# Optimization experiments

Hardware: AMD Instinct MI355X
Metric: run time of the kernel (lower is better)

The kernel has to match this reference:

```python
import jax, jax.numpy as jnp
import numpy as np

TEMPORAL_WIDTH = 4  # hardcoded in GRUBlock


def causal_conv1d(x, w, b):
    """Depthwise causal temporal conv. x:[B,T,R], w:[4,R], b:[R].
    out[t] = sum_i w[i] * x[t - 3 + i] + b (zero left padding)."""
    T = x.shape[1]
    xp = jnp.pad(x, ((0, 0), (TEMPORAL_WIDTH - 1, 0), (0, 0)))
    y = b
    for i in range(TEMPORAL_WIDTH):  # tiny fixed loop over 4 taps
        y = y + w[i] * xp[:, i:i + T]
    return y


def linear_scan(a, b):
    """h_t = a_t * h_{t-1} + b_t with h_{-1}=0, via associative scan over time."""
    def comb(e1, e2):
        a1, b1 = e1
        a2, b2 = e2
        return a2 * a1, a2 * b1 + b2
    _, h = jax.lax.associative_scan(comb, (a, b), axis=1)
    return h


def setup_inputs() -> dict:
    key = jax.random.key(0)
    k1, k2, k3, k4 = jax.random.split(key, 4)
    B, T, H, R = 4, 8192, 1024, 1024
    x = jax.random.normal(k1, (B, T, H), dtype=jnp.float32)
    # lecun init: N(0, 1/sqrt(d_in)); torch Linear weight is [out, in]
    w_zh = jax.random.normal(k2, (2 * R, H), dtype=jnp.float32) / np.sqrt(H)
    w_out = jax.random.normal(k3, (H, R), dtype=jnp.float32) / np.sqrt(R)
    conv_w = jax.random.normal(k4, (TEMPORAL_WIDTH, R), dtype=jnp.float32) / np.sqrt(TEMPORAL_WIDTH)
    conv_b = jnp.zeros((R,), dtype=jnp.float32)
    return {"x": x, "w_zh": w_zh, "w_out": w_out, "conv_w": conv_w, "conv_b": conv_b}


def reference(x, w_zh, w_out, conv_w, conv_b):
    # residual causal conv
    x = x + causal_conv1d(x, conv_w, conv_b)
    # fused z/h projection: [B,T,H] @ [H,2R]
    zh = jnp.einsum('bth,rh->btr', x, w_zh)
    z, h = jnp.split(zh, 2, axis=-1)
    z = jax.nn.sigmoid(z)
    # GRU-style linear recurrence: h_t = (1-z_t) h_{t-1} + z_t h~_t
    h_o = linear_scan(1.0 - z, z * h)
    return jnp.einsum('btr,hr->bth', h_o, w_out)
```

## Files before the change

kernel.cpp:

```cpp
#include <hip/hip_runtime.h>

typedef __bf16 bf16x8 __attribute__((ext_vector_type(8)));
typedef __bf16 bf16x4 __attribute__((ext_vector_type(4)));
typedef float  f32x4  __attribute__((ext_vector_type(4)));

static constexpr int Bb = 4, T = 8192, H = 1024, R = 1024;
static constexpr int BT = Bb * T;
static constexpr int N1 = 2 * R;
static constexpr int CH = 64;
static constexpr int L  = T / CH;

__device__ __forceinline__ void g2lds16(const void* g, void* l) {
  __builtin_amdgcn_global_load_lds(
      (const __attribute__((address_space(1))) unsigned int*)g,
      (__attribute__((address_space(3))) unsigned int*)l, 16, 0, 0);
}

__global__ __launch_bounds__(256) void cast_f32_bf16(const float* __restrict__ in,
                                                     __bf16* __restrict__ out, int n4) {
  int i = blockIdx.x * 256 + threadIdx.x;
  if (i >= n4) return;
  const f32x4 v = *(const f32x4*)(in + (size_t)i * 4);
  bf16x4 o;
  o[0] = (__bf16)v[0]; o[1] = (__bf16)v[1]; o[2] = (__bf16)v[2]; o[3] = (__bf16)v[3];
  *(bf16x4*)(out + (size_t)i * 4) = o;
}

__global__ __launch_bounds__(256) void conv_residual_cast(const float* __restrict__ x,
                                                          const float* __restrict__ cw,
                                                          const float* __restrict__ cb,
                                                          __bf16* __restrict__ xc) {
  const size_t i4 = (size_t)blockIdx.x * 256 + threadIdx.x;
  const size_t v  = i4 * 4;
  const int    h  = (int)(v & (size_t)(H - 1));
  const size_t bt = v >> 10;
  const int    t  = (int)(bt & (size_t)(T - 1));
  f32x4 acc = *(const f32x4*)(cb + h);
  const f32x4 xv = *(const f32x4*)(x + v);
#pragma unroll
  for (int i = 0; i < 4; ++i) {
    const int tt = t - 3 + i;
    if (tt >= 0) {
      const f32x4 xi = *(const f32x4*)(x + (bt - 3 + i) * H + h);
      const f32x4 wi = *(const f32x4*)(cw + i * H + h);
      acc += wi * xi;
    }
  }
  acc += xv;
  bf16x4 o;
  o[0] = (__bf16)acc[0]; o[1] = (__bf16)acc[1]; o[2] = (__bf16)acc[2]; o[3] = (__bf16)acc[3];
  *(bf16x4*)(xc + v) = o;
}

template <typename OUT_T>
__global__ __launch_bounds__(256) void gemm_bt(const __bf16* __restrict__ A,
                                               const __bf16* __restrict__ Bm,
                                               OUT_T* __restrict__ C,
                                               int M, int N, int K) {
  __shared__ __align__(16) __bf16 sA[128 * 32];
  __shared__ __align__(16) __bf16 sB[128 * 32];
  const int tid  = threadIdx.x;
  const int wave = tid >> 6;
  const int lane = tid & 63;
  const int lr = lane & 15;
  const int lq = lane >> 4;
  const int bm0 = blockIdx.y * 128;
  const int bn0 = blockIdx.x * 128;
  const int wm = (wave >> 1) * 64;
  const int wn = (wave & 1) * 64;

  f32x4 acc[4][4] = {};

  const size_t aBase = (size_t)(bm0 + (tid >> 2)) * K + (tid & 3) * 8;
  const size_t bBase = (size_t)(bn0 + (tid >> 2)) * K + (tid & 3) * 8;
  const int ldsOff = (tid & ~63) * 8;

  for (int k0 = 0; k0 < K; k0 += 32) {
    g2lds16(A  + aBase + k0,                 sA + ldsOff);
    g2lds16(A  + aBase + (size_t)64 * K + k0, sA + ldsOff + 2048);
    g2lds16(Bm + bBase + k0,                 sB + ldsOff);
    g2lds16(Bm + bBase + (size_t)64 * K + k0, sB + ldsOff + 2048);
    __syncthreads();
    bf16x8 af[4], bfr[4];
#pragma unroll
    for (int i = 0; i < 4; ++i) {
      af[i]  = *(const bf16x8*)(sA + (wm + i * 16 + lr) * 32 + lq * 8);
      bfr[i] = *(const bf16x8*)(sB + (wn + i * 16 + lr) * 32 + lq * 8);
    }
#pragma unroll
    for (int i = 0; i < 4; ++i)
#pragma unroll
      for (int j = 0; j < 4; ++j)
        acc[i][j] = __builtin_amdgcn_mfma_f32_16x16x32_bf16(af[i], bfr[j], acc[i][j], 0, 0, 0);
    __syncthreads();
  }
#pragma unroll
  for (int i = 0; i < 4; ++i)
#pragma unroll
    for (int j = 0; j < 4; ++j) {
      const int col = bn0 + wn + j * 16 + lr;
#pragma unroll
      for (int rr = 0; rr < 4; ++rr) {
        const int row = bm0 + wm + i * 16 + lq * 4 + rr;
        C[(size_t)row * N + col] = (OUT_T)acc[i][j][rr];
      }
    }
}

__global__ __launch_bounds__(256) void scan_pass1(const __bf16* __restrict__ zh,
                                                  float* __restrict__ aggA,
                                                  float* __restrict__ aggB) {
  const int r = blockIdx.x * 256 + threadIdx.x;
  const int c = blockIdx.y;
  const int b = blockIdx.z;
  size_t base = ((size_t)b * T + (size_t)c * L) * N1 + r;
  float Aacc = 1.f, Bacc = 0.f;
#pragma unroll 4
  for (int t = 0; t < L; ++t) {
    const float s  = (float)zh[base];
    const float hh = (float)zh[base + R];
    base += N1;
    const float z = 1.f / (1.f + __expf(-s));
    const float a = 1.f - z;
    Bacc = a * Bacc + z * hh;
    Aacc *= a;
  }
  const size_t o = ((size_t)b * CH + c) * R + r;
  aggA[o] = Aacc;
  aggB[o] = Bacc;
}

__global__ __launch_bounds__(256) void scan_pass2(const float* __restrict__ aggA,
                                                  const float* __restrict__ aggB,
                                                  float* __restrict__ carry) {
  const int idx = blockIdx.x * 256 + threadIdx.x;
  const int b = idx >> 10;
  const int r = idx & (R - 1);
  float h = 0.f;
#pragma unroll 8
  for (int c = 0; c < CH; ++c) {
    const size_t o = ((size_t)b * CH + c) * R + r;
    carry[o] = h;
    h = aggA[o] * h + aggB[o];
  }
}

__global__ __launch_bounds__(256) void scan_pass3(const __bf16* __restrict__ zh,
                                                  const float* __restrict__ carry,
                                                  __bf16* __restrict__ ho) {
  const int r = blockIdx.x * 256 + threadIdx.x;
  const int c = blockIdx.y;
  const int b = blockIdx.z;
  size_t base  = ((size_t)b * T + (size_t)c * L) * N1 + r;
  size_t obase = ((size_t)b * T + (size_t)c * L) * R + r;
  float h = carry[((size_t)b * CH + c) * R + r];
#pragma unroll 4
  for (int t = 0; t < L; ++t) {
    const float s  = (float)zh[base];
    const float hh = (float)zh[base + R];
    base += N1;
    const float z = 1.f / (1.f + __expf(-s));
    h = (1.f - z) * h + z * hh;
    ho[obase] = (__bf16)h;
    obase += R;
  }
}

extern "C" void kernel_launch(void* const* d_in, const int* in_sizes, int n_in,
                              void* d_out, int out_size, void* d_ws, size_t ws_size,
                              hipStream_t stream) {
  const float* x      = (const float*)d_in[0];
  const float* w_zh   = (const float*)d_in[1];
  const float* w_out  = (const float*)d_in[2];
  const float* conv_w = (const float*)d_in[3];
  const float* conv_b = (const float*)d_in[4];
  float* out = (float*)d_out;

  char* ws = (char*)d_ws;
  size_t off = 0;
  __bf16* wzh_b  = (__bf16*)(ws + off); off += (size_t)N1 * H * 2;
  __bf16* wout_b = (__bf16*)(ws + off); off += (size_t)H * R * 2;
  __bf16* xc     = (__bf16*)(ws + off); off += (size_t)BT * H * 2;
  __bf16* zh     = (__bf16*)(ws + off); off += (size_t)BT * N1 * 2;
  float*  aggA   = (float*)(ws + off);  off += (size_t)Bb * CH * R * 4;
  float*  aggB   = (float*)(ws + off);  off += (size_t)Bb * CH * R * 4;
  float*  carry  = (float*)(ws + off);  off += (size_t)Bb * CH * R * 4;
  __bf16* ho = xc;

  cast_f32_bf16<<<(N1 * H / 4 + 255) / 256, 256, 0, stream>>>(w_zh, wzh_b, N1 * H / 4);
  cast_f32_bf16<<<(H * R / 4 + 255) / 256, 256, 0, stream>>>(w_out, wout_b, H * R / 4);
  conv_residual_cast<<<BT * H / 4 / 256, 256, 0, stream>>>(x, conv_w, conv_b, xc);
  gemm_bt<__bf16><<<dim3(N1 / 128, BT / 128), 256, 0, stream>>>(xc, wzh_b, zh, BT, N1, H);
  scan_pass1<<<dim3(R / 256, CH, Bb), 256, 0, stream>>>(zh, aggA, aggB);
  scan_pass2<<<Bb * R / 256, 256, 0, stream>>>(aggA, aggB, carry);
  scan_pass3<<<dim3(R / 256, CH, Bb), 256, 0, stream>>>(zh, carry, ho);
  gemm_bt<float><<<dim3(H / 128, BT / 128), 256, 0, stream>>>(ho, wout_b, out, BT, H, R);
}
```

Measured before the change: 649.5 us.

## Use 32x32x16 MFMA with BK=64 and XOR-swizzled LDS in GEMM

Rewrites the bf16 GEMM inner loop to use 32x32x16 MFMA instructions instead of 16x16x32, doubles the K-tile to 64 so there are half as many barrier pairs per K, and XOR-swizzles the LDS layout to avoid bank conflicts on the fragment reads. The larger MFMA needs fewer LDS fragment loads per flop, and the bigger K step amortizes synchronization. In exchange it doubles LDS use per block and carries more complex index arithmetic, with a new output row mapping that has to match the 32x32 accumulator layout.

```diff
diff --git a/kernel.cpp b/kernel.cpp
--- a/kernel.cpp
+++ b/kernel.cpp
@@ -3,6 +3,7 @@
 typedef __bf16 bf16x8 __attribute__((ext_vector_type(8)));
 typedef __bf16 bf16x4 __attribute__((ext_vector_type(4)));
 typedef float  f32x4  __attribute__((ext_vector_type(4)));
+typedef float  f32x16 __attribute__((ext_vector_type(16)));
 
 static constexpr int Bb = 4, T = 8192, H = 1024, R = 1024;
 static constexpr int BT = Bb * T;
@@ -57,51 +58,62 @@
                                                const __bf16* __restrict__ Bm,
                                                OUT_T* __restrict__ C,
                                                int M, int N, int K) {
-  __shared__ __align__(16) __bf16 sA[128 * 32];
-  __shared__ __align__(16) __bf16 sB[128 * 32];
+  __shared__ __align__(16) __bf16 sA[128 * 64];
+  __shared__ __align__(16) __bf16 sB[128 * 64];
   const int tid  = threadIdx.x;
   const int wave = tid >> 6;
   const int lane = tid & 63;
-  const int lr = lane & 15;
-  const int lq = lane >> 4;
+  const int ln = lane & 31;
+  const int kb = lane >> 5;
   const int bm0 = blockIdx.y * 128;
   const int bn0 = blockIdx.x * 128;
   const int wm = (wave >> 1) * 64;
   const int wn = (wave & 1) * 64;
 
-  f32x4 acc[4][4] = {};
-
-  const size_t aBase = (size_t)(bm0 + (tid >> 2)) * K + (tid & 3) * 8;
-  const size_t bBase = (size_t)(bn0 + (tid >> 2)) * K + (tid & 3) * 8;
-  const int ldsOff = (tid & ~63) * 8;
-
-  for (int k0 = 0; k0 < K; k0 += 32) {
-    g2lds16(A  + aBase + k0,                 sA + ldsOff);
-    g2lds16(A  + aBase + (size_t)64 * K + k0, sA + ldsOff + 2048);
-    g2lds16(Bm + bBase + k0,                 sB + ldsOff);
-    g2lds16(Bm + bBase + (size_t)64 * K + k0, sB + ldsOff + 2048);
+  f32x16 acc[2][2] = {};
+
+  int srow[4], sgc[4], sldsE[4];
+#pragma unroll
+  for (int c = 0; c < 4; ++c) {
+    const int li = c * 256 + tid;
+    srow[c] = li >> 3;
+    sgc[c]  = (li & 7) ^ (srow[c] & 7);
+    sldsE[c] = (c * 256 + (tid & ~63)) * 8;
+  }
+
+  for (int k0 = 0; k0 < K; k0 += 64) {
+#pragma unroll
+    for (int c = 0; c < 4; ++c) {
+      g2lds16(A  + (size_t)(bm0 + srow[c]) * K + k0 + sgc[c] * 8, sA + sldsE[c]);
+      g2lds16(Bm + (size_t)(bn0 + srow[c]) * K + k0 + sgc[c] * 8, sB + sldsE[c]);
+    }
     __syncthreads();
-    bf16x8 af[4], bfr[4];
-#pragma unroll
-    for (int i = 0; i < 4; ++i) {
-      af[i]  = *(const bf16x8*)(sA + (wm + i * 16 + lr) * 32 + lq * 8);
-      bfr[i] = *(const bf16x8*)(sB + (wn + i * 16 + lr) * 32 + lq * 8);
-    }
-#pragma unroll
-    for (int i = 0; i < 4; ++i)
-#pragma unroll
-      for (int j = 0; j < 4; ++j)
-        acc[i][j] = __builtin_amdgcn_mfma_f32_16x16x32_bf16(af[i], bfr[j], acc[i][j], 0, 0, 0);
+#pragma unroll
+    for (int ks = 0; ks < 4; ++ks) {
+      bf16x8 af[2], bfr[2];
+#pragma unroll
+      for (int i = 0; i < 2; ++i) {
+        const int ra = wm + i * 32 + ln;
+        af[i]  = *(const bf16x8*)(sA + ra * 64 + (((2 * ks + kb) ^ (ra & 7)) * 8));
+        const int rb = wn + i * 32 + ln;
+        bfr[i] = *(const bf16x8*)(sB + rb * 64 + (((2 * ks + kb) ^ (rb & 7)) * 8));
+      }
+#pragma unroll
+      for (int i = 0; i < 2; ++i)
+#pragma unroll
+        for (int j = 0; j < 2; ++j)
+          acc[i][j] = __builtin_amdgcn_mfma_f32_32x32x16_bf16(af[i], bfr[j], acc[i][j], 0, 0, 0);
+    }
     __syncthreads();
   }
 #pragma unroll
-  for (int i = 0; i < 4; ++i)
-#pragma unroll
-    for (int j = 0; j < 4; ++j) {
-      const int col = bn0 + wn + j * 16 + lr;
-#pragma unroll
-      for (int rr = 0; rr < 4; ++rr) {
-        const int row = bm0 + wm + i * 16 + lq * 4 + rr;
+  for (int i = 0; i < 2; ++i)
+#pragma unroll
+    for (int j = 0; j < 2; ++j) {
+      const int col = bn0 + wn + j * 32 + ln;
+#pragma unroll
+      for (int rr = 0; rr < 16; ++rr) {
+        const int row = bm0 + wm + i * 32 + (rr & 3) + 8 * (rr >> 2) + 4 * kb;
         C[(size_t)row * N + col] = (OUT_T)acc[i][j][rr];
       }
     }
```

After: 609.3 us. -6.2%, faster.
